# Performance work log

Hardware: AMD Instinct MI355X
Metric: run time of the kernel (lower is better)

## Reference

```python
import jax, jax.numpy as jnp
import numpy as np

D_MODEL = 1024
NUM_HEADS = 16
D_K = D_MODEL // NUM_HEADS
THETA = 10000.0
MAX_SEQ_LEN = 2048
B, S = 2, 2048


def _rope(x, positions):
    """Apply interleaved RoPE. x: [B,H,S,dk], positions: [B,S]."""
    dim_idx = jnp.arange(D_K // 2, dtype=jnp.float32)
    freqs = 1.0 / (THETA ** (2.0 * dim_idx / D_K))          # [dk/2]
    angles = positions.astype(jnp.float32)[..., None] * freqs  # [B,S,dk/2]
    cos = jnp.cos(angles)[:, None, :, :]                     # [B,1,S,dk/2]
    sin = jnp.sin(angles)[:, None, :, :]
    x_even = x[..., 0::2]
    x_odd = x[..., 1::2]
    out_even = cos * x_even - sin * x_odd
    out_odd = sin * x_even + cos * x_odd
    return jnp.stack([out_even, out_odd], axis=-1).reshape(x.shape)


def setup_inputs() -> dict:
    key = jax.random.key(0)
    k1, k2, k3, k4 = jax.random.split(key, 4)
    x = jax.random.normal(k1, (B, S, D_MODEL), dtype=jnp.float32)
    token_positions = jnp.sort(
        jax.random.randint(k2, (B, S), 0, MAX_SEQ_LEN), axis=-1
    ).astype(jnp.int32)
    W_qkv = jax.random.normal(k3, (3 * D_MODEL, D_MODEL), dtype=jnp.float32) * 0.02
    W_o = jax.random.normal(k4, (D_MODEL, D_MODEL), dtype=jnp.float32) * 0.02
    return {"x": x, "token_positions": token_positions, "W_qkv": W_qkv, "W_o": W_o}


def reference(x, token_positions, W_qkv, W_o):
    # fused QKV projection: [B,S,3*D]
    qkv = jnp.einsum('bsd,ed->bse', x, W_qkv)
    qkv = qkv.reshape(B, S, 3, NUM_HEADS, D_K)
    qkv = jnp.transpose(qkv, (0, 2, 3, 1, 4))  # [B,3,H,S,dk]
    Q, K, V = qkv[:, 0], qkv[:, 1], qkv[:, 2]  # each [B,H,S,dk]

    Q = _rope(Q, token_positions)
    K = _rope(K, token_positions)

    # causal scaled dot-product attention
    scores = jnp.einsum('bhqd,bhkd->bhqk', Q, K) / jnp.sqrt(jnp.float32(D_K))
    causal = jnp.tril(jnp.ones((S, S), dtype=bool))
    scores = jnp.where(causal, scores, jnp.float32(-1e30))
    attn = jax.nn.softmax(scores, axis=-1)
    out = jnp.einsum('bhqk,bhkd->bhqd', attn, V)  # [B,H,S,dk]

    out = jnp.transpose(out, (0, 2, 1, 3)).reshape(B, S, D_MODEL)
    return jnp.einsum('bsd,ed->bse', out, W_o)
```

## Files before the change

### kernel.cpp

```cpp
#include <hip/hip_runtime.h>
#include <hip/hip_bf16.h>


using u16 = unsigned short;
typedef __attribute__((ext_vector_type(8))) short short8;
typedef __attribute__((ext_vector_type(4))) float f32x4;
typedef __attribute__((ext_vector_type(16))) float f32x16;
typedef __attribute__((ext_vector_type(2))) unsigned uint2v;
typedef __attribute__((ext_vector_type(4))) unsigned uint4v;

__device__ __forceinline__ float bf2f(u16 v) {
  unsigned u = ((unsigned)v) << 16; float f; __builtin_memcpy(&f, &u, 4); return f;
}
__device__ __forceinline__ u16 f2bf(float f) {
  unsigned u; __builtin_memcpy(&u, &f, 4);
  return (u16)((u + 0x7fffu + ((u >> 16) & 1u)) >> 16);
}
__device__ __forceinline__ float u2f(unsigned u) {
  float f; __builtin_memcpy(&f, &u, 4); return f;
}
__device__ __forceinline__ unsigned f2u(float f) {
  unsigned u; __builtin_memcpy(&u, &f, 4); return u;
}
__device__ __forceinline__ float xhalf_max(float x) {
  uint2v s = __builtin_amdgcn_permlane32_swap(f2u(x), f2u(x), false, false);
  unsigned ax = s.x, bx = s.y;
  return fmaxf(u2f(ax), u2f(bx));
}
__device__ __forceinline__ float xhalf_sum(float x) {
  uint2v s = __builtin_amdgcn_permlane32_swap(f2u(x), f2u(x), false, false);
  unsigned ax = s.x, bx = s.y;
  return u2f(ax) + u2f(bx);
}

__device__ __forceinline__ void gload_lds16(const void* g, void* l) {
  __builtin_amdgcn_global_load_lds((const __attribute__((address_space(1))) unsigned*)g,
                                   (__attribute__((address_space(3))) unsigned*)l, 16, 0, 0);
}

__global__ __launch_bounds__(256) void cvt_all(const float* __restrict__ x, const float* __restrict__ wqkv,
                                               const float* __restrict__ wo, u16* __restrict__ xb,
                                               u16* __restrict__ wqkvb, u16* __restrict__ wob) {
  int i = blockIdx.x * 256 + threadIdx.x;
  const float* src; u16* dst; int off;
  if (i < 1048576) { src = x; dst = xb; off = i; }
  else if (i < 1048576 + 786432) { src = wqkv; dst = wqkvb; off = i - 1048576; }
  else { src = wo; dst = wob; off = i - (1048576 + 786432); }
  float4 v = *(const float4*)(src + (size_t)off * 4);
  unsigned lo = f2bf(v.x) | ((unsigned)f2bf(v.y) << 16);
  unsigned hi = f2bf(v.z) | ((unsigned)f2bf(v.w) << 16);
  uint2 w; w.x = lo; w.y = hi;
  *(uint2*)(dst + (size_t)off * 4) = w;
}

template <typename OutT>
__global__ __launch_bounds__(256) void gemm_bt2(const u16* __restrict__ A, const u16* __restrict__ B,
                                                OutT* __restrict__ C, int M, int N, int K) {
  __shared__ u16 As[128 * 64];
  __shared__ u16 Bs[128 * 64];
  const int tid = threadIdx.x;
  const int wave = tid >> 6;
  const int lane = tid & 63;
  const int m0 = blockIdx.x * 128;
  const int n0 = blockIdx.y * 128;
  const int wm = (wave >> 1) * 64;
  const int wn = (wave & 1) * 64;

  f32x4 acc[4][4];
#pragma unroll
  for (int m = 0; m < 4; ++m)
#pragma unroll
    for (int n = 0; n < 4; ++n) acc[m][n] = (f32x4){0.f, 0.f, 0.f, 0.f};

  const int srow = lane >> 3;
  const int sslot = lane & 7;
  const int fr = lane & 15;
  const int fk = lane >> 4;

  for (int k0 = 0; k0 < K; k0 += 64) {
    __syncthreads();
#pragma unroll
    for (int q = 0; q < 4; ++q) {
      int r = wave * 32 + q * 8 + srow;
      int src_slot = sslot ^ (r & 7);
      gload_lds16(A + (size_t)(m0 + r) * K + k0 + src_slot * 8, As + r * 64 + sslot * 8);
      gload_lds16(B + (size_t)(n0 + r) * K + k0 + src_slot * 8, Bs + r * 64 + sslot * 8);
    }
    __syncthreads();

#pragma unroll
    for (int kk = 0; kk < 2; ++kk) {
      short8 af[4], bf[4];
#pragma unroll
      for (int m = 0; m < 4; ++m) {
        int r = wm + m * 16 + fr;
        af[m] = *(const short8*)(As + r * 64 + (((kk * 4 + fk) ^ (r & 7)) << 3));
      }
#pragma unroll
      for (int n = 0; n < 4; ++n) {
        int r = wn + n * 16 + fr;
        bf[n] = *(const short8*)(Bs + r * 64 + (((kk * 4 + fk) ^ (r & 7)) << 3));
      }
#pragma unroll
      for (int m = 0; m < 4; ++m)
#pragma unroll
        for (int n = 0; n < 4; ++n)
          acc[m][n] = __builtin_amdgcn_mfma_f32_16x16x32_bf16(af[m], bf[n], acc[m][n], 0, 0, 0);
    }
  }

  const int fg = lane >> 4;
#pragma unroll
  for (int m = 0; m < 4; ++m)
#pragma unroll
    for (int n = 0; n < 4; ++n)
#pragma unroll
      for (int r = 0; r < 4; ++r) {
        int row = m0 + wm + m * 16 + fg * 4 + r;
        int col = n0 + wn + n * 16 + fr;
        if constexpr (sizeof(OutT) == 2)
          C[(size_t)row * N + col] = (OutT)f2bf(acc[m][n][r]);
        else
          C[(size_t)row * N + col] = (OutT)acc[m][n][r];
      }
}

template <typename OutT>
__global__ __launch_bounds__(256) void gemm_bt64_2(const u16* __restrict__ A, const u16* __restrict__ B,
                                                   OutT* __restrict__ C, int M, int N, int K) {
  __shared__ u16 As[64 * 64];
  __shared__ u16 Bs[128 * 64];
  const int tid = threadIdx.x;
  const int wave = tid >> 6;
  const int lane = tid & 63;
  const int m0 = blockIdx.x * 64;
  const int n0 = blockIdx.y * 128;
  const int wm = (wave >> 1) * 32;
  const int wn = (wave & 1) * 64;

  f32x4 acc[2][4];
#pragma unroll
  for (int m = 0; m < 2; ++m)
#pragma unroll
    for (int n = 0; n < 4; ++n) acc[m][n] = (f32x4){0.f, 0.f, 0.f, 0.f};

  const int srow = lane >> 3;
  const int sslot = lane & 7;
  const int fr = lane & 15;
  const int fk = lane >> 4;

  for (int k0 = 0; k0 < K; k0 += 64) {
    __syncthreads();
#pragma unroll
    for (int q = 0; q < 2; ++q) {
      int r = wave * 16 + q * 8 + srow;
      int src_slot = sslot ^ (r & 7);
      gload_lds16(A + (size_t)(m0 + r) * K + k0 + src_slot * 8, As + r * 64 + sslot * 8);
    }
#pragma unroll
    for (int q = 0; q < 4; ++q) {
      int r = wave * 32 + q * 8 + srow;
      int src_slot = sslot ^ (r & 7);
      gload_lds16(B + (size_t)(n0 + r) * K + k0 + src_slot * 8, Bs + r * 64 + sslot * 8);
    }
    __syncthreads();

#pragma unroll
    for (int kk = 0; kk < 2; ++kk) {
      short8 af[2], bf[4];
#pragma unroll
      for (int m = 0; m < 2; ++m) {
        int r = wm + m * 16 + fr;
        af[m] = *(const short8*)(As + r * 64 + (((kk * 4 + fk) ^ (r & 7)) << 3));
      }
#pragma unroll
      for (int n = 0; n < 4; ++n) {
        int r = wn + n * 16 + fr;
        bf[n] = *(const short8*)(Bs + r * 64 + (((kk * 4 + fk) ^ (r & 7)) << 3));
      }
#pragma unroll
      for (int m = 0; m < 2; ++m)
#pragma unroll
        for (int n = 0; n < 4; ++n)
          acc[m][n] = __builtin_amdgcn_mfma_f32_16x16x32_bf16(af[m], bf[n], acc[m][n], 0, 0, 0);
    }
  }

  const int fg = lane >> 4;
#pragma unroll
  for (int m = 0; m < 2; ++m)
#pragma unroll
    for (int n = 0; n < 4; ++n)
#pragma unroll
      for (int r = 0; r < 4; ++r) {
        int row = m0 + wm + m * 16 + fg * 4 + r;
        int col = n0 + wn + n * 16 + fr;
        if constexpr (sizeof(OutT) == 2)
          C[(size_t)row * N + col] = (OutT)f2bf(acc[m][n][r]);
        else
          C[(size_t)row * N + col] = (OutT)acc[m][n][r];
      }
}

__global__ __launch_bounds__(256) void rope_qk2(const u16* __restrict__ qkv, const int* __restrict__ pos,
                                                u16* __restrict__ Qf, u16* __restrict__ Kf) {
  int t = blockIdx.x * 256 + threadIdx.x;
  int l = t & 63;
  int j = (t >> 6) & 3;
  int tile = (t >> 8) & 63;
  int bh = t >> 14;
  int b = bh >> 4, h = bh & 15;
  int s = tile * 32 + (l & 31);
  int dbase = j * 16 + (l >> 5) * 8;
  float p = (float)pos[(b << 11) + s];
  const u16* src = qkv + ((size_t)((b << 11) + s)) * 3072 + h * 64 + dbase;
  uint4 qv = *(const uint4*)src;
  uint4 kv = *(const uint4*)(src + 1024);
  unsigned qin[4] = {qv.x, qv.y, qv.z, qv.w};
  unsigned kin[4] = {kv.x, kv.y, kv.z, kv.w};
  unsigned qo[4], ko[4];
  const float QS = 0.18033688011112043f;
#pragma unroll
  for (int kp = 0; kp < 4; ++kp) {
    int i = (dbase >> 1) + kp;
    float ang = p * __builtin_exp2f(-(float)i * 0.41524101186f);
    float sn, cs;
    sincosf(ang, &sn, &cs);
    float qe = bf2f((u16)(qin[kp] & 0xffff)), qd = bf2f((u16)(qin[kp] >> 16));
    float ke = bf2f((u16)(kin[kp] & 0xffff)), kd = bf2f((u16)(kin[kp] >> 16));
    qo[kp] = f2bf((cs * qe - sn * qd) * QS) | ((unsigned)f2bf((sn * qe + cs * qd) * QS) << 16);
    ko[kp] = f2bf(cs * ke - sn * kd) | ((unsigned)f2bf(sn * ke + cs * kd) << 16);
  }
  size_t o = ((((size_t)bh * 64 + tile) * 4 + j) * 64 + l) * 8;
  uint4 qw; qw.x = qo[0]; qw.y = qo[1]; qw.z = qo[2]; qw.w = qo[3];
  uint4 kw; kw.x = ko[0]; kw.y = ko[1]; kw.z = ko[2]; kw.w = ko[3];
  *(uint4*)(Qf + o) = qw;
  *(uint4*)(Kf + o) = kw;
}

__global__ __launch_bounds__(256) void v_pack(const u16* __restrict__ qkv, u16* __restrict__ Vf) {
  __shared__ u16 lds[64][72];
  const int bh = blockIdx.y;
  const int b = bh >> 4, h = bh & 15;
  const int s0 = blockIdx.x * 64;
  const int t = threadIdx.x;
  {
    const int r = t >> 3;
    const int c = t & 7;
#pragma unroll
    for (int p = 0; p < 2; ++p) {
      int s = r + p * 32;
      const u16* src = qkv + ((size_t)((b << 11) + s0 + s)) * 3072 + 2048 + h * 64 + c * 8;
      *(uint4*)&lds[s][c * 8] = *(const uint4*)src;
    }
  }
  __syncthreads();
#pragma unroll
  for (int p = 0; p < 2; ++p) {
    int item = t + p * 256;
    int tt = item >> 8;
    int seg = (item >> 6) & 3;
    int l = item & 63;
    int d = (seg >> 1) * 32 + (l & 31);
    int sb = tt * 32 + (seg & 1) * 16 + (l >> 5) * 8;
    u16 tmp[8];
#pragma unroll
    for (int e = 0; e < 8; ++e) tmp[e] = lds[sb + e][d];
    int kt = (s0 >> 5) + tt;
    size_t o = ((((size_t)bh * 64 + kt) * 4 + seg) * 64 + l) * 8;
    *(uint4*)(Vf + o) = *(uint4*)tmp;
  }
}

__global__ __launch_bounds__(256, 2) void attn6(const u16* __restrict__ Qf, const u16* __restrict__ Kf,
                                                const u16* __restrict__ Vf, u16* __restrict__ Ao) {
  __shared__ float smM[3][64], smL[3][64];
  __shared__ float smO[3][64][33];
  const int tid = threadIdx.x;
  const int lane = tid & 63;
  const int wid = tid >> 6;
  const int bid = blockIdx.x;
  const int xcd = bid & 7;
  const int rr = bid >> 3;
  const int bh = xcd * 4 + (rr & 3);
  const int qt = 63 - (rr >> 2);
  const int q0 = qt * 32;
  const u16* __restrict__ Qp = Qf + (size_t)bh * 131072;
  const u16* __restrict__ Kp = Kf + (size_t)bh * 131072;
  const u16* __restrict__ Vp = Vf + (size_t)bh * 131072;
  const int lq = lane & 31;
  const int hi = lane >> 5;

  const u16* qb = Qp + (size_t)qt * 2048 + lane * 8;
  short8 qf0 = *(const short8*)(qb);
  short8 qf1 = *(const short8*)(qb + 512);
  short8 qf2 = *(const short8*)(qb + 1024);
  short8 qf3 = *(const short8*)(qb + 1536);

  f32x16 o0, o1;
#pragma unroll
  for (int r = 0; r < 16; ++r) { o0[r] = 0.f; o1[r] = 0.f; }
  float m = -1e30f, lsum = 0.f;

  const int nkt = qt + 1;
  const int base = nkt >> 2, rem = nkt & 3;
  const int cnt = base + (wid < rem ? 1 : 0);
  const int beg = wid * base + (wid < rem ? wid : rem);

  if (cnt > 0) {
    const u16* kp = Kp + (size_t)beg * 2048 + lane * 8;
    const u16* vp = Vp + (size_t)beg * 2048 + lane * 8;
    short8 kc0 = *(const short8*)(kp);
    short8 kc1 = *(const short8*)(kp + 512);
    short8 kc2 = *(const short8*)(kp + 1024);
    short8 kc3 = *(const short8*)(kp + 1536);
    short8 vc0 = *(const short8*)(vp);
    short8 vc1 = *(const short8*)(vp + 512);
    short8 vc2 = *(const short8*)(vp + 1024);
    short8 vc3 = *(const short8*)(vp + 1536);

    for (int i = 0; i < cnt; ++i) {
      const int kt = beg + i;
      const int ktn = beg + (i + 1 < cnt ? i + 1 : i);
      const u16* kpn = Kp + (size_t)ktn * 2048 + lane * 8;
      const u16* vpn = Vp + (size_t)ktn * 2048 + lane * 8;
      short8 kn0 = *(const short8*)(kpn);
      short8 kn1 = *(const short8*)(kpn + 512);
      short8 kn2 = *(const short8*)(kpn + 1024);
      short8 kn3 = *(const short8*)(kpn + 1536);
      short8 vn0 = *(const short8*)(vpn);
      short8 vn1 = *(const short8*)(vpn + 512);
      short8 vn2 = *(const short8*)(vpn + 1024);
      short8 vn3 = *(const short8*)(vpn + 1536);

      f32x16 sc;
#pragma unroll
      for (int r = 0; r < 16; ++r) sc[r] = 0.f;
      sc = __builtin_amdgcn_mfma_f32_32x32x16_bf16(kc0, qf0, sc, 0, 0, 0);
      sc = __builtin_amdgcn_mfma_f32_32x32x16_bf16(kc1, qf1, sc, 0, 0, 0);
      sc = __builtin_amdgcn_mfma_f32_32x32x16_bf16(kc2, qf2, sc, 0, 0, 0);
      sc = __builtin_amdgcn_mfma_f32_32x32x16_bf16(kc3, qf3, sc, 0, 0, 0);

      if (kt == qt) {
#pragma unroll
        for (int r = 0; r < 16; ++r) {
          int ko = (r & 3) + 8 * (r >> 2) + 4 * hi;
          sc[r] = (ko <= lq) ? sc[r] : -1e30f;
        }
      }

      float t0 = fmaxf(fmaxf(sc[0], sc[1]), sc[2]);
      float t1 = fmaxf(fmaxf(sc[3], sc[4]), sc[5]);
      float t2 = fmaxf(fmaxf(sc[6], sc[7]), sc[8]);
      float t3 = fmaxf(fmaxf(sc[9], sc[10]), sc[11]);
      float t4 = fmaxf(fmaxf(sc[12], sc[13]), sc[14]);
      float t5 = fmaxf(fmaxf(t0, t1), sc[15]);
      float t6 = fmaxf(fmaxf(t2, t3), t4);
      float pmax = xhalf_max(fmaxf(t5, t6));

      if (!__all(pmax - m <= 11.5f)) {
        float nm = fmaxf(m, pmax);
        float alpha = __builtin_exp2f(m - nm);
        lsum *= alpha;
#pragma unroll
        for (int r = 0; r < 16; ++r) { o0[r] *= alpha; o1[r] *= alpha; }
        m = nm;
      }

#pragma unroll
      for (int r = 0; r < 16; ++r) sc[r] = __builtin_exp2f(sc[r] - m);
      float r8[8];
#pragma unroll
      for (int r = 0; r < 8; ++r) r8[r] = sc[r] + sc[r + 8];
#pragma unroll
      for (int s = 4; s >= 1; s >>= 1)
#pragma unroll
        for (int r = 0; r < s; ++r) r8[r] += r8[r + s];
      lsum += xhalf_sum(r8[0]);

      unsigned w[8];
#pragma unroll
      for (int t = 0; t < 8; ++t) {
        unsigned d;
        asm("v_cvt_pk_bf16_f32 %0, %1, %2" : "=v"(d) : "v"(sc[2 * t]), "v"(sc[2 * t + 1]));
        w[t] = d;
      }
      short8 pb0, pb1;
      {
        uint2v r1 = __builtin_amdgcn_permlane32_swap(w[0], w[2], false, false);
        uint2v r2 = __builtin_amdgcn_permlane32_swap(w[1], w[3], false, false);
        unsigned r1x = r1.x, r1y = r1.y, r2x = r2.x, r2y = r2.y;
        uint4v t4v; t4v.x = r1x; t4v.y = r2x; t4v.z = r1y; t4v.w = r2y;
        pb0 = __builtin_bit_cast(short8, t4v);
        uint2v r3 = __builtin_amdgcn_permlane32_swap(w[4], w[6], false, false);
        uint2v r4 = __builtin_amdgcn_permlane32_swap(w[5], w[7], false, false);
        unsigned r3x = r3.x, r3y = r3.y, r4x = r4.x, r4y = r4.y;
        uint4v t5v; t5v.x = r3x; t5v.y = r4x; t5v.z = r3y; t5v.w = r4y;
        pb1 = __builtin_bit_cast(short8, t5v);
      }

      o0 = __builtin_amdgcn_mfma_f32_32x32x16_bf16(vc0, pb0, o0, 0, 0, 0);
      o0 = __builtin_amdgcn_mfma_f32_32x32x16_bf16(vc1, pb1, o0, 0, 0, 0);
      o1 = __builtin_amdgcn_mfma_f32_32x32x16_bf16(vc2, pb0, o1, 0, 0, 0);
      o1 = __builtin_amdgcn_mfma_f32_32x32x16_bf16(vc3, pb1, o1, 0, 0, 0);

      kc0 = kn0; kc1 = kn1; kc2 = kn2; kc3 = kn3;
      vc0 = vn0; vc1 = vn1; vc2 = vn2; vc3 = vn3;
    }
  }

  if (wid != 0) {
    smM[wid - 1][lane] = m;
    smL[wid - 1][lane] = lsum;
#pragma unroll
    for (int r = 0; r < 16; ++r) smO[wid - 1][lane][r] = o0[r];
#pragma unroll
    for (int r = 0; r < 16; ++r) smO[wid - 1][lane][16 + r] = o1[r];
  }
  __syncthreads();
  if (wid == 0) {
    float m1 = smM[0][lane], m2 = smM[1][lane], m3 = smM[2][lane];
    float M = fmaxf(fmaxf(m, m1), fmaxf(m2, m3));
    float a0 = __builtin_exp2f(m - M);
    float a1 = __builtin_exp2f(m1 - M);
    float a2 = __builtin_exp2f(m2 - M);
    float a3 = __builtin_exp2f(m3 - M);
    float L = lsum * a0 + smL[0][lane] * a1 + smL[1][lane] * a2 + smL[2][lane] * a3;
    float inv = 1.f / L;
    const int b = bh >> 4, h = bh & 15;
    u16* outp = Ao + ((size_t)(b << 11) + q0 + lq) * 1024 + h * 64;
#pragma unroll
    for (int g = 0; g < 4; ++g) {
      int d = 8 * g + 4 * hi;
      float c[8];
#pragma unroll
      for (int j = 0; j < 4; ++j) {
        c[j] = (o0[4 * g + j] * a0 + smO[0][lane][4 * g + j] * a1 +
                smO[1][lane][4 * g + j] * a2 + smO[2][lane][4 * g + j] * a3) * inv;
        c[4 + j] = (o1[4 * g + j] * a0 + smO[0][lane][16 + 4 * g + j] * a1 +
                    smO[1][lane][16 + 4 * g + j] * a2 + smO[2][lane][16 + 4 * g + j] * a3) * inv;
      }
      uint2v w0;
      w0.x = f2bf(c[0]) | ((unsigned)f2bf(c[1]) << 16);
      w0.y = f2bf(c[2]) | ((unsigned)f2bf(c[3]) << 16);
      *(uint2v*)(outp + d) = w0;
      uint2v w1;
      w1.x = f2bf(c[4]) | ((unsigned)f2bf(c[5]) << 16);
      w1.y = f2bf(c[6]) | ((unsigned)f2bf(c[7]) << 16);
      *(uint2v*)(outp + 32 + d) = w1;
    }
  }
}

extern "C" void kernel_launch(void* const* d_in, const int* in_sizes, int n_in,
                              void* d_out, int out_size, void* d_ws, size_t ws_size,
                              hipStream_t stream) {
  const float* x = (const float*)d_in[0];
  const int* pos = (const int*)d_in[1];
  const float* Wqkv = (const float*)d_in[2];
  const float* Wo = (const float*)d_in[3];
  float* out = (float*)d_out;

  char* ws = (char*)d_ws;
  const size_t MB = 1024 * 1024;
  u16* xb     = (u16*)(ws);
  u16* wqkvb  = (u16*)(ws + 8 * MB);
  u16* wob    = (u16*)(ws + 14 * MB);
  u16* qkv    = (u16*)(ws + 16 * MB);
  u16* Qf     = (u16*)(ws + 40 * MB);
  u16* Kf     = (u16*)(ws + 48 * MB);
  u16* Vf     = (u16*)(ws + 56 * MB);
  u16* ao     = (u16*)(ws + 64 * MB);

  cvt_all<<<8192, 256, 0, stream>>>(x, Wqkv, Wo, xb, wqkvb, wob);
  gemm_bt2<u16><<<dim3(32, 24), 256, 0, stream>>>(xb, wqkvb, qkv, 4096, 3072, 1024);
  rope_qk2<<<2048, 256, 0, stream>>>(qkv, pos, Qf, Kf);
  v_pack<<<dim3(32, 32), 256, 0, stream>>>(qkv, Vf);
  attn6<<<2048, 256, 0, stream>>>(Qf, Kf, Vf, ao);
  gemm_bt64_2<float><<<dim3(64, 8), 256, 0, stream>>>(ao, wob, out, 4096, 1024, 1024);
}
```

Before: 179.3 us.

## Fuse RoPE and Q/K/V packing into the QKV projection GEMM epilogue

```diff
diff --git a/kernel.cpp b/kernel.cpp
--- a/kernel.cpp
+++ b/kernel.cpp
@@ -53,11 +53,12 @@
   *(uint2*)(dst + (size_t)off * 4) = w;
 }
 
-template <typename OutT>
-__global__ __launch_bounds__(256) void gemm_bt2(const u16* __restrict__ A, const u16* __restrict__ B,
-                                                OutT* __restrict__ C, int M, int N, int K) {
+__global__ __launch_bounds__(256) void gemm_qkv_fused(const u16* __restrict__ A, const u16* __restrict__ B,
+                                                      const int* __restrict__ pos, u16* __restrict__ Qf,
+                                                      u16* __restrict__ Kf, u16* __restrict__ Vf) {
   __shared__ u16 As[128 * 64];
   __shared__ u16 Bs[128 * 64];
+  const int K = 1024;
   const int tid = threadIdx.x;
   const int wave = tid >> 6;
   const int lane = tid & 63;
@@ -76,6 +77,7 @@
   const int sslot = lane & 7;
   const int fr = lane & 15;
   const int fk = lane >> 4;
+  const int fg = lane >> 4;
 
   for (int k0 = 0; k0 < K; k0 += 64) {
     __syncthreads();
@@ -109,20 +111,64 @@
     }
   }
 
-  const int fg = lane >> 4;
-#pragma unroll
-  for (int m = 0; m < 4; ++m)
-#pragma unroll
-    for (int n = 0; n < 4; ++n)
-#pragma unroll
-      for (int r = 0; r < 4; ++r) {
-        int row = m0 + wm + m * 16 + fg * 4 + r;
-        int col = n0 + wn + n * 16 + fr;
-        if constexpr (sizeof(OutT) == 2)
-          C[(size_t)row * N + col] = (OutT)f2bf(acc[m][n][r]);
-        else
-          C[(size_t)row * N + col] = (OutT)acc[m][n][r];
-      }
+  const int h = ((n0 + wn) >> 6) & 15;
+  const int ny = blockIdx.y;
+
+  if (ny < 16) {
+    u16* __restrict__ dst = (ny < 8) ? Qf : Kf;
+    const float scale = (ny < 8) ? 0.18033688011112043f : 1.0f;
+#pragma unroll
+    for (int n = 0; n < 4; ++n) {
+      const int d = n * 16 + fr;
+      const float f = __builtin_exp2f(-(float)(d >> 1) * 0.41524101186f);
+      const int j = n;
+      const int lofs = 32 * (fr >> 3);
+      const int e = fr & 7;
+#pragma unroll
+      for (int m = 0; m < 4; ++m) {
+        const int t = ((m0 + wm + m * 16) >> 5) & 63;
+#pragma unroll
+        for (int r = 0; r < 4; ++r) {
+          const int sg = m0 + wm + m * 16 + fg * 4 + r;
+          float p = (float)pos[sg];
+          float sn, cs;
+          __sincosf(p * f, &sn, &cs);
+          float v = acc[m][n][r];
+          float vpart = __shfl_xor(v, 1);
+          float oe = (cs * v - sn * vpart) * scale;
+          float oo = (sn * v + cs * vpart) * scale;
+          if (!(fr & 1)) {
+            unsigned w = f2bf(oe) | ((unsigned)f2bf(oo) << 16);
+            int bh = ((sg >> 11) << 4) + h;
+            *(unsigned*)(dst + (size_t)bh * 131072 + t * 2048 + j * 512 +
+                         ((sg & 31) + lofs) * 8 + e) = w;
+          }
+        }
+      }
+    }
+  } else {
+#pragma unroll
+    for (int n = 0; n < 4; ++n) {
+      const int d = n * 16 + fr;
+      const int seg_hi = (d >> 5) << 1;
+      const int l = (d & 31) + 32 * (fg >> 1);
+#pragma unroll
+      for (int m = 0; m < 4; ++m) {
+        const int sgb = m0 + wm + m * 16;
+        const int t = (sgb >> 5) & 63;
+        const int seg = seg_hi | (m & 1);
+        unsigned lo = f2bf(acc[m][n][0]) | ((unsigned)f2bf(acc[m][n][1]) << 16);
+        unsigned hi2 = f2bf(acc[m][n][2]) | ((unsigned)f2bf(acc[m][n][3]) << 16);
+        unsigned plo = __shfl_xor(lo, 16);
+        unsigned phi = __shfl_xor(hi2, 16);
+        if (!(fg & 1)) {
+          int bh = ((sgb >> 11) << 4) + h;
+          uint4 w; w.x = lo; w.y = hi2; w.z = plo; w.w = phi;
+          *(uint4*)(Vf + (size_t)bh * 131072 + t * 2048 + seg * 512 + l * 8) = w;
+        }
+      }
+    }
+  }
 }
 
 template <typename OutT>
@@ -200,76 +246,6 @@
         else
           C[(size_t)row * N + col] = (OutT)acc[m][n][r];
       }
-}
-
-__global__ __launch_bounds__(256) void rope_qk2(const u16* __restrict__ qkv, const int* __restrict__ pos,
-                                                u16* __restrict__ Qf, u16* __restrict__ Kf) {
-  int t = blockIdx.x * 256 + threadIdx.x;
-  int l = t & 63;
-  int j = (t >> 6) & 3;
-  int tile = (t >> 8) & 63;
-  int bh = t >> 14;
-  int b = bh >> 4, h = bh & 15;
-  int s = tile * 32 + (l & 31);
-  int dbase = j * 16 + (l >> 5) * 8;
-  float p = (float)pos[(b << 11) + s];
-  const u16* src = qkv + ((size_t)((b << 11) + s)) * 3072 + h * 64 + dbase;
-  uint4 qv = *(const uint4*)src;
-  uint4 kv = *(const uint4*)(src + 1024);
-  unsigned qin[4] = {qv.x, qv.y, qv.z, qv.w};
-  unsigned kin[4] = {kv.x, kv.y, kv.z, kv.w};
-  unsigned qo[4], ko[4];
-  const float QS = 0.18033688011112043f;
-#pragma unroll
-  for (int kp = 0; kp < 4; ++kp) {
-    int i = (dbase >> 1) + kp;
-    float ang = p * __builtin_exp2f(-(float)i * 0.41524101186f);
-    float sn, cs;
-    sincosf(ang, &sn, &cs);
-    float qe = bf2f((u16)(qin[kp] & 0xffff)), qd = bf2f((u16)(qin[kp] >> 16));
-    float ke = bf2f((u16)(kin[kp] & 0xffff)), kd = bf2f((u16)(kin[kp] >> 16));
-    qo[kp] = f2bf((cs * qe - sn * qd) * QS) | ((unsigned)f2bf((sn * qe + cs * qd) * QS) << 16);
-    ko[kp] = f2bf(cs * ke - sn * kd) | ((unsigned)f2bf(sn * ke + cs * kd) << 16);
-  }
-  size_t o = ((((size_t)bh * 64 + tile) * 4 + j) * 64 + l) * 8;
-  uint4 qw; qw.x = qo[0]; qw.y = qo[1]; qw.z = qo[2]; qw.w = qo[3];
-  uint4 kw; kw.x = ko[0]; kw.y = ko[1]; kw.z = ko[2]; kw.w = ko[3];
-  *(uint4*)(Qf + o) = qw;
-  *(uint4*)(Kf + o) = kw;
-}
-
-__global__ __launch_bounds__(256) void v_pack(const u16* __restrict__ qkv, u16* __restrict__ Vf) {
-  __shared__ u16 lds[64][72];
-  const int bh = blockIdx.y;
-  const int b = bh >> 4, h = bh & 15;
-  const int s0 = blockIdx.x * 64;
-  const int t = threadIdx.x;
-  {
-    const int r = t >> 3;
-    const int c = t & 7;
-#pragma unroll
-    for (int p = 0; p < 2; ++p) {
-      int s = r + p * 32;
-      const u16* src = qkv + ((size_t)((b << 11) + s0 + s)) * 3072 + 2048 + h * 64 + c * 8;
-      *(uint4*)&lds[s][c * 8] = *(const uint4*)src;
-    }
-  }
-  __syncthreads();
-#pragma unroll
-  for (int p = 0; p < 2; ++p) {
-    int item = t + p * 256;
-    int tt = item >> 8;
-    int seg = (item >> 6) & 3;
-    int l = item & 63;
-    int d = (seg >> 1) * 32 + (l & 31);
-    int sb = tt * 32 + (seg & 1) * 16 + (l >> 5) * 8;
-    u16 tmp[8];
-#pragma unroll
-    for (int e = 0; e < 8; ++e) tmp[e] = lds[sb + e][d];
-    int kt = (s0 >> 5) + tt;
-    size_t o = ((((size_t)bh * 64 + kt) * 4 + seg) * 64 + l) * 8;
-    *(uint4*)(Vf + o) = *(uint4*)tmp;
-  }
 }
 
 __global__ __launch_bounds__(256, 2) void attn6(const u16* __restrict__ Qf, const u16* __restrict__ Kf,
@@ -336,10 +312,12 @@
       f32x16 sc;
 #pragma unroll
       for (int r = 0; r < 16; ++r) sc[r] = 0.f;
+      __builtin_amdgcn_s_setprio(1);
       sc = __builtin_amdgcn_mfma_f32_32x32x16_bf16(kc0, qf0, sc, 0, 0, 0);
       sc = __builtin_amdgcn_mfma_f32_32x32x16_bf16(kc1, qf1, sc, 0, 0, 0);
       sc = __builtin_amdgcn_mfma_f32_32x32x16_bf16(kc2, qf2, sc, 0, 0, 0);
       sc = __builtin_amdgcn_mfma_f32_32x32x16_bf16(kc3, qf3, sc, 0, 0, 0);
+      __builtin_amdgcn_s_setprio(0);
 
       if (kt == qt) {
 #pragma unroll
@@ -399,10 +377,12 @@
         pb1 = __builtin_bit_cast(short8, t5v);
       }
 
+      __builtin_amdgcn_s_setprio(1);
       o0 = __builtin_amdgcn_mfma_f32_32x32x16_bf16(vc0, pb0, o0, 0, 0, 0);
       o0 = __builtin_amdgcn_mfma_f32_32x32x16_bf16(vc1, pb1, o0, 0, 0, 0);
       o1 = __builtin_amdgcn_mfma_f32_32x32x16_bf16(vc2, pb0, o1, 0, 0, 0);
       o1 = __builtin_amdgcn_mfma_f32_32x32x16_bf16(vc3, pb1, o1, 0, 0, 0);
+      __builtin_amdgcn_s_setprio(0);
 
       kc0 = kn0; kc1 = kn1; kc2 = kn2; kc3 = kn3;
       vc0 = vn0; vc1 = vn1; vc2 = vn2; vc3 = vn3;
@@ -466,16 +446,13 @@
   u16* xb     = (u16*)(ws);
   u16* wqkvb  = (u16*)(ws + 8 * MB);
   u16* wob    = (u16*)(ws + 14 * MB);
-  u16* qkv    = (u16*)(ws + 16 * MB);
-  u16* Qf     = (u16*)(ws + 40 * MB);
-  u16* Kf     = (u16*)(ws + 48 * MB);
-  u16* Vf     = (u16*)(ws + 56 * MB);
-  u16* ao     = (u16*)(ws + 64 * MB);
+  u16* Qf     = (u16*)(ws + 16 * MB);
+  u16* Kf     = (u16*)(ws + 24 * MB);
+  u16* Vf     = (u16*)(ws + 32 * MB);
+  u16* ao     = (u16*)(ws + 40 * MB);
 
   cvt_all<<<8192, 256, 0, stream>>>(x, Wqkv, Wo, xb, wqkvb, wob);
-  gemm_bt2<u16><<<dim3(32, 24), 256, 0, stream>>>(xb, wqkvb, qkv, 4096, 3072, 1024);
-  rope_qk2<<<2048, 256, 0, stream>>>(qkv, pos, Qf, Kf);
-  v_pack<<<dim3(32, 32), 256, 0, stream>>>(qkv, Vf);
+  gemm_qkv_fused<<<dim3(32, 24), 256, 0, stream>>>(xb, wqkvb, pos, Qf, Kf, Vf);
   attn6<<<2048, 256, 0, stream>>>(Qf, Kf, Vf, ao);
   gemm_bt64_2<float><<<dim3(64, 8), 256, 0, stream>>>(ao, wob, out, 4096, 1024, 1024);
 }
```

Result: slower. 188.2 us (+5.0%).
